# Performance work log

Measured on AMD Instinct MI355X. Metric: run time of the kernel, lower is better.

Reference implementation:

```python
import jax, jax.numpy as jnp
import numpy as np

DIM = 1024
N_HEADS = 16
HEAD_DIM = DIM // N_HEADS
LN_EPS = 1e-5


def layer_norm(x, gamma, beta):
    mu = jnp.mean(x, axis=-1, keepdims=True)
    var = jnp.var(x, axis=-1, keepdims=True)
    return (x - mu) * jax.lax.rsqrt(var + LN_EPS) * gamma + beta


def setup_inputs() -> dict:
    key = jax.random.key(0)
    ks = jax.random.split(key, 12)
    B, Nq, Nc, D = 2, 2048, 2048, DIM
    s = 1.0 / np.sqrt(D)
    return {
        "query": jax.random.normal(ks[0], (B, Nq, D), jnp.float32),
        "context": jax.random.normal(ks[1], (B, Nc, D), jnp.float32),
        "Wq": jax.random.normal(ks[2], (D, D), jnp.float32) * s,
        "bq": jnp.zeros((D,), jnp.float32),
        "Wk": jax.random.normal(ks[3], (D, D), jnp.float32) * s,
        "bk": jnp.zeros((D,), jnp.float32),
        "Wv": jax.random.normal(ks[4], (D, D), jnp.float32) * s,
        "bv": jnp.zeros((D,), jnp.float32),
        "Wo": jax.random.normal(ks[5], (D, D), jnp.float32) * s,
        "bo": jnp.zeros((D,), jnp.float32),
        "gq": jnp.ones((D,), jnp.float32),
        "betaq": jnp.zeros((D,), jnp.float32),
        "gkv": jnp.ones((D,), jnp.float32),
        "betakv": jnp.zeros((D,), jnp.float32),
    }


def reference(query, context, Wq, bq, Wk, bk, Wv, bv, Wo, bo, gq, betaq, gkv, betakv):
    B, Nq, D = query.shape
    Nc = context.shape[1]
    residual = query
    q = layer_norm(query, gq, betaq)
    c = layer_norm(context, gkv, betakv)
    # projections; (B,N,D) -> (B,H,N,hd)
    Q = (q @ Wq + bq).reshape(B, Nq, N_HEADS, HEAD_DIM).transpose(0, 2, 1, 3)
    K = (c @ Wk + bk).reshape(B, Nc, N_HEADS, HEAD_DIM).transpose(0, 2, 1, 3)
    V = (c @ Wv + bv).reshape(B, Nc, N_HEADS, HEAD_DIM).transpose(0, 2, 1, 3)
    scores = jnp.einsum("bhqd,bhkd->bhqk", Q, K) / np.sqrt(HEAD_DIM).astype(np.float32)
    attn = jax.nn.softmax(scores, axis=-1)
    out = jnp.einsum("bhqk,bhkd->bhqd", attn, V)
    out = out.transpose(0, 2, 1, 3).reshape(B, Nq, D)
    return residual + out @ Wo + bo
```

## Files before the change

### kernel.cpp

```cpp
#include <hip/hip_runtime.h>
#include <hip/hip_bf16.h>

typedef unsigned short u16;
typedef unsigned long long u64;
typedef __bf16 bf16x8 __attribute__((ext_vector_type(8)));
typedef float f32x4 __attribute__((ext_vector_type(4)));
typedef float f32x16 __attribute__((ext_vector_type(16)));
typedef unsigned u32x4 __attribute__((ext_vector_type(4)));

#define DIM 1024
#define NH 16
#define HD 64
#define QSCALE 0.180336880972788f

__device__ __forceinline__ u16 f2bf(float f) {
  union { float f; unsigned u; } v; v.f = f;
  unsigned r = v.u + 0x7fffu + ((v.u >> 16) & 1u);
  return (u16)(r >> 16);
}

__device__ __forceinline__ unsigned pk2(float a, float b) {
  union { __hip_bfloat162 h; unsigned u; } cv;
  cv.h = __float22bfloat162_rn(make_float2(a, b));
  return cv.u;
}

__device__ __forceinline__ float bf2f(unsigned s) {
  union { unsigned u; float f; } v; v.u = s << 16; return v.f;
}

__device__ __forceinline__ float fexp2(float x) {
#if __has_builtin(__builtin_amdgcn_exp2f)
  return __builtin_amdgcn_exp2f(x);
#else
  return exp2f(x);
#endif
}

__device__ __forceinline__ void gld16(const u16* gp, u16* lp) {
  __builtin_amdgcn_global_load_lds(
      (const __attribute__((address_space(1))) unsigned int*)(const void*)gp,
      (__attribute__((address_space(3))) unsigned int*)(void*)lp, 16, 0, 0);
}

__device__ __forceinline__ void pl32swap(unsigned& a, unsigned& b) {
  asm volatile("v_permlane32_swap_b32 %0, %1" : "+v"(a), "+v"(b));
}

__device__ __forceinline__ void drain_vm_barrier() {
  asm volatile("s_waitcnt vmcnt(0)" ::: "memory");
  __builtin_amdgcn_s_barrier();
}

__global__ __launch_bounds__(256) void prep_kernel(
    const float* __restrict__ q, const float* __restrict__ c,
    const float* __restrict__ gq, const float* __restrict__ bq,
    const float* __restrict__ gkv, const float* __restrict__ bkv,
    u16* __restrict__ qn, u16* __restrict__ cn,
    const float* W0, const float* W1, const float* W2, const float* W3,
    u16* O0, u16* O1, u16* O2, u16* O3) {
  __shared__ float red[2][4];
  __shared__ float t[32][33];
  int bid = blockIdx.x, tid = threadIdx.x;
  if (bid < 8192) {
    const float* x  = bid < 4096 ? q : c;
    const float* g  = bid < 4096 ? gq : gkv;
    const float* be = bid < 4096 ? bq : bkv;
    u16* out = bid < 4096 ? qn : cn;
    int row = bid & 4095;
    float4 v = ((const float4*)(x + (size_t)row * DIM))[tid];
    float s1 = v.x + v.y + v.z + v.w;
    float s2 = v.x * v.x + v.y * v.y + v.z * v.z + v.w * v.w;
#pragma unroll
    for (int o = 32; o >= 1; o >>= 1) { s1 += __shfl_xor(s1, o, 64); s2 += __shfl_xor(s2, o, 64); }
    int wv = tid >> 6;
    if ((tid & 63) == 0) { red[0][wv] = s1; red[1][wv] = s2; }
    __syncthreads();
    s1 = red[0][0] + red[0][1] + red[0][2] + red[0][3];
    s2 = red[1][0] + red[1][1] + red[1][2] + red[1][3];
    float mu = s1 * (1.f / DIM);
    float var = s2 * (1.f / DIM) - mu * mu;
    float rs = rsqrtf(var + 1e-5f);
    float4 gv = ((const float4*)g)[tid];
    float4 bv = ((const float4*)be)[tid];
    uint2 o2;
    o2.x = pk2((v.x - mu) * rs * gv.x + bv.x, (v.y - mu) * rs * gv.y + bv.y);
    o2.y = pk2((v.z - mu) * rs * gv.z + bv.z, (v.w - mu) * rs * gv.w + bv.w);
    ((uint2*)(out + (size_t)row * DIM))[tid] = o2;
  } else {
    int wid = bid - 8192;
    int z = wid >> 10;
    const float* W = z == 0 ? W0 : z == 1 ? W1 : z == 2 ? W2 : W3;
    u16* O        = z == 0 ? O0 : z == 1 ? O1 : z == 2 ? O2 : O3;
    int xy = wid & 1023;
    int bx = (xy & 31) * 32, by = (xy >> 5) * 32;
    int tx = tid & 31, ty = tid >> 5;
#pragma unroll
    for (int i = 0; i < 4; ++i) t[ty + i * 8][tx] = W[(size_t)(by + ty + i * 8) * DIM + bx + tx];
    __syncthreads();
#pragma unroll
    for (int i = 0; i < 4; ++i) O[(size_t)(bx + ty + i * 8) * DIM + by + tx] = f2bf(t[tx][ty + i * 8]);
  }
}

#define QKV_BUF 16384
__global__ __launch_bounds__(256) void gemm_qkv(
    const u16* __restrict__ qn, const u16* __restrict__ cn,
    const u16* __restrict__ Wqt, const u16* __restrict__ Wkt, const u16* __restrict__ Wvt,
    const float* __restrict__ bq, const float* __restrict__ bk, const float* __restrict__ bv,
    u16* __restrict__ Qb, u16* __restrict__ Kb, u16* __restrict__ Vtb) {
  __shared__ __align__(16) u16 sm[2 * QKV_BUF];
  int tid = threadIdx.x, wave = tid >> 6, lane = tid & 63;
  int lr = lane & 15, quad = lane >> 4;
  int m0 = blockIdx.x * 128, n0 = blockIdx.y * 64;
  int wm = (wave >> 1) * 64, wn = (wave & 1) * 32;

  if (blockIdx.z == 0) {
    auto stage = [&](int buf, int kt) {
      u16* As  = sm + buf * QKV_BUF;
      u16* B0s = As + 128 * 64;
      u16* B1s = As + 192 * 64;
#pragma unroll
      for (int r = 0; r < 4; ++r) {
        int slot = tid + r * 256;
        int row = slot >> 3;
        int c = (slot & 7) ^ (row & 7);
        gld16(cn + (size_t)(m0 + row) * DIM + kt + c * 8, &As[slot * 8]);
      }
#pragma unroll
      for (int r = 0; r < 2; ++r) {
        int slot = tid + r * 256;
        int row = slot >> 3;
        int c = (slot & 7) ^ (row & 7);
        gld16(Wkt + (size_t)(n0 + row) * DIM + kt + c * 8, &B0s[slot * 8]);
        gld16(Wvt + (size_t)(n0 + row) * DIM + kt + c * 8, &B1s[slot * 8]);
      }
    };

    f32x4 acck[4][2] = {}, accv[4][2] = {};
    stage(0, 0);
    drain_vm_barrier();
    int cur = 0;
    for (int kt = 0; kt < DIM; kt += 64) {
      if (kt + 64 < DIM) stage(cur ^ 1, kt + 64);
      const u16* As  = sm + cur * QKV_BUF;
      const u16* B0s = As + 128 * 64;
      const u16* B1s = As + 192 * 64;
#pragma unroll
      for (int kc = 0; kc < 2; ++kc) {
        int pc = ((kc * 4 + quad) ^ (lr & 7)) * 8;
        bf16x8 af[4], b0f[2], b1f[2];
#pragma unroll
        for (int i = 0; i < 4; ++i) af[i] = *(const bf16x8*)&As[(wm + i * 16 + lr) * 64 + pc];
#pragma unroll
        for (int j = 0; j < 2; ++j) {
          b0f[j] = *(const bf16x8*)&B0s[(wn + j * 16 + lr) * 64 + pc];
          b1f[j] = *(const bf16x8*)&B1s[(wn + j * 16 + lr) * 64 + pc];
        }
#pragma unroll
        for (int mi = 0; mi < 4; ++mi)
#pragma unroll
          for (int ni = 0; ni < 2; ++ni) {
            acck[mi][ni] = __builtin_amdgcn_mfma_f32_16x16x32_bf16(af[mi], b0f[ni], acck[mi][ni], 0, 0, 0);
            accv[mi][ni] = __builtin_amdgcn_mfma_f32_16x16x32_bf16(b1f[ni], af[mi], accv[mi][ni], 0, 0, 0);
          }
      }
      drain_vm_barrier();
      cur ^= 1;
    }
#pragma unroll
    for (int mi = 0; mi < 4; ++mi)
#pragma unroll
      for (int ni = 0; ni < 2; ++ni) {
        int col = n0 + wn + ni * 16 + lr;
        float bb_ = bk[col];
        int row0 = m0 + wm + mi * 16 + quad * 4;
#pragma unroll
        for (int r = 0; r < 4; ++r)
          Kb[(size_t)(row0 + r) * DIM + col] = f2bf(acck[mi][ni][r] + bb_);
      }
#pragma unroll
    for (int mi = 0; mi < 4; ++mi) {
      int m = m0 + wm + mi * 16 + lr;
      int bb = m >> 11, tt = m & 2047;
      u16* outb = Vtb + (((size_t)bb << 10)) * 2048 + tt;
#pragma unroll
      for (int ni = 0; ni < 2; ++ni) {
        int nbase = n0 + wn + ni * 16 + quad * 4;
#pragma unroll
        for (int r = 0; r < 4; ++r)
          outb[(size_t)(nbase + r) * 2048] = f2bf(accv[mi][ni][r] + bv[nbase + r]);
      }
    }
  } else {
    auto stage = [&](int buf, int kt) {
      u16* As  = sm + buf * QKV_BUF;
      u16* B0s = As + 128 * 64;
#pragma unroll
      for (int r = 0; r < 4; ++r) {
        int slot = tid + r * 256;
        int row = slot >> 3;
        int c = (slot & 7) ^ (row & 7);
        gld16(qn + (size_t)(m0 + row) * DIM + kt + c * 8, &As[slot * 8]);
      }
#pragma unroll
      for (int r = 0; r < 2; ++r) {
        int slot = tid + r * 256;
        int row = slot >> 3;
        int c = (slot & 7) ^ (row & 7);
        gld16(Wqt + (size_t)(n0 + row) * DIM + kt + c * 8, &B0s[slot * 8]);
      }
    };

    f32x4 acc[4][2] = {};
    stage(0, 0);
    drain_vm_barrier();
    int cur = 0;
    for (int kt = 0; kt < DIM; kt += 64) {
      if (kt + 64 < DIM) stage(cur ^ 1, kt + 64);
      const u16* As  = sm + cur * QKV_BUF;
      const u16* B0s = As + 128 * 64;
#pragma unroll
      for (int kc = 0; kc < 2; ++kc) {
        int pc = ((kc * 4 + quad) ^ (lr & 7)) * 8;
        bf16x8 af[4], b0f[2];
#pragma unroll
        for (int i = 0; i < 4; ++i) af[i] = *(const bf16x8*)&As[(wm + i * 16 + lr) * 64 + pc];
#pragma unroll
        for (int j = 0; j < 2; ++j) b0f[j] = *(const bf16x8*)&B0s[(wn + j * 16 + lr) * 64 + pc];
#pragma unroll
        for (int mi = 0; mi < 4; ++mi)
#pragma unroll
          for (int ni = 0; ni < 2; ++ni)
            acc[mi][ni] = __builtin_amdgcn_mfma_f32_16x16x32_bf16(af[mi], b0f[ni], acc[mi][ni], 0, 0, 0);
      }
      drain_vm_barrier();
      cur ^= 1;
    }
#pragma unroll
    for (int mi = 0; mi < 4; ++mi)
#pragma unroll
      for (int ni = 0; ni < 2; ++ni) {
        int col = n0 + wn + ni * 16 + lr;
        float bb_ = bq[col];
        int row0 = m0 + wm + mi * 16 + quad * 4;
#pragma unroll
        for (int r = 0; r < 4; ++r)
          Qb[(size_t)(row0 + r) * DIM + col] = f2bf((acc[mi][ni][r] + bb_) * QSCALE);
      }
  }
}

#define O_BUF 12288
__global__ __launch_bounds__(256) void gemm_o(const u16* __restrict__ A,
    const u16* __restrict__ Bt, const float* __restrict__ bias,
    float* __restrict__ out, const float* __restrict__ resid) {
  __shared__ __align__(16) u16 sm[2 * O_BUF];
  int tid = threadIdx.x, wave = tid >> 6, lane = tid & 63;
  int lr = lane & 15, quad = lane >> 4;
  int m0 = blockIdx.x * 128, n0 = blockIdx.y * 64;
  int wm = (wave >> 1) * 64, wn = (wave & 1) * 32;

  auto stage = [&](int buf, int kt) {
    u16* As = sm + buf * O_BUF;
    u16* Bs = As + 128 * 64;
#pragma unroll
    for (int r = 0; r < 4; ++r) {
      int slot = tid + r * 256;
      int row = slot >> 3;
      int c = (slot & 7) ^ (row & 7);
      gld16(A + (size_t)(m0 + row) * DIM + kt + c * 8, &As[slot * 8]);
    }
#pragma unroll
    for (int r = 0; r < 2; ++r) {
      int slot = tid + r * 256;
      int row = slot >> 3;
      int c = (slot & 7) ^ (row & 7);
      gld16(Bt + (size_t)(n0 + row) * DIM + kt + c * 8, &Bs[slot * 8]);
    }
  };

  f32x4 acc[4][2] = {};
  stage(0, 0);
  drain_vm_barrier();
  int cur = 0;
  for (int kt = 0; kt < DIM; kt += 64) {
    if (kt + 64 < DIM) stage(cur ^ 1, kt + 64);
    const u16* As = sm + cur * O_BUF;
    const u16* Bs = As + 128 * 64;
#pragma unroll
    for (int kc = 0; kc < 2; ++kc) {
      int pc = ((kc * 4 + quad) ^ (lr & 7)) * 8;
      bf16x8 af[4], bfr[2];
#pragma unroll
      for (int i = 0; i < 4; ++i) af[i] = *(const bf16x8*)&As[(wm + i * 16 + lr) * 64 + pc];
#pragma unroll
      for (int j = 0; j < 2; ++j) bfr[j] = *(const bf16x8*)&Bs[(wn + j * 16 + lr) * 64 + pc];
#pragma unroll
      for (int mi = 0; mi < 4; ++mi)
#pragma unroll
        for (int ni = 0; ni < 2; ++ni)
          acc[mi][ni] = __builtin_amdgcn_mfma_f32_16x16x32_bf16(af[mi], bfr[ni], acc[mi][ni], 0, 0, 0);
    }
    drain_vm_barrier();
    cur ^= 1;
  }
#pragma unroll
  for (int mi = 0; mi < 4; ++mi)
#pragma unroll
    for (int ni = 0; ni < 2; ++ni) {
      int col = n0 + wn + ni * 16 + lr;
      float bv = bias[col];
      int row0 = m0 + wm + mi * 16 + quad * 4;
#pragma unroll
      for (int r = 0; r < 4; ++r) {
        int row = row0 + r;
        out[(size_t)row * DIM + col] = acc[mi][ni][r] + bv + resid[(size_t)row * DIM + col];
      }
    }
}

__global__ __launch_bounds__(256, 4) void flash_kernel(const u16* __restrict__ Q,
    const u16* __restrict__ Kg, const u16* __restrict__ Vt,
    u16* __restrict__ O0, u16* __restrict__ O1,
    float* __restrict__ L0, float* __restrict__ L1) {
  __shared__ __align__(16) u16 lds[16384];
  int tid = threadIdx.x, wave = tid >> 6, lane = tid & 63;
  int ln = lane & 31, hi = lane >> 5;
  int bh = blockIdx.x, b = bh >> 4, h = bh & 15;
  int q0 = blockIdx.y * 128;
  int split = blockIdx.z;
  u16* Op = split ? O1 : O0;
  float* Lp = split ? L1 : L0;
  int t0 = split * 1024;

  const u16* kbase = Kg + (size_t)(b * 2048 + t0) * DIM + h * HD;
  const u16* vbase = Vt + (size_t)(b * 1024 + h * HD) * 2048 + t0;

  size_t qrow = (size_t)(b * 2048 + q0 + wave * 32 + ln);
  bf16x8 qf[4];
#pragma unroll
  for (int ds = 0; ds < 4; ++ds)
    qf[ds] = *(const bf16x8*)&Q[qrow * DIM + h * HD + ds * 16 + hi * 8];

  int slot0 = tid, slot1 = tid + 256;
  int r0 = slot0 >> 3, c0 = (slot0 & 7) ^ (r0 & 7);
  int r1 = slot1 >> 3, c1 = (slot1 & 7) ^ (r1 & 7);
  const u16* kp0 = kbase + (size_t)r0 * DIM + c0 * 8;
  const u16* kp1 = kbase + (size_t)r1 * DIM + c1 * 8;
  const u16* vp0 = vbase + (size_t)r0 * 2048 + c0 * 8;
  const u16* vp1 = vbase + (size_t)r1 * 2048 + c1 * 8;

  gld16(kp0, &lds[slot0 * 8]);
  gld16(kp1, &lds[slot1 * 8]);
  gld16(vp0, &lds[8192 + slot0 * 8]);
  gld16(vp1, &lds[8192 + slot1 * 8]);
  __syncthreads();

  float plsum = 0.f;
  f32x16 oacc[2] = {};

  for (int j = 0; j < 16; ++j) {
    int par = j & 1;
    const u16* kcb = &lds[par * 4096];
    const u16* vcb = &lds[8192 + par * 4096];

    f32x16 sf[2] = {};
    __builtin_amdgcn_s_setprio(1);
#pragma unroll
    for (int kt2 = 0; kt2 < 2; ++kt2) {
      int rs = (kt2 * 32 + ln) * 64;
      int rx = (kt2 * 32 + ln) & 7;
#pragma unroll
      for (int ds = 0; ds < 4; ++ds) {
        bf16x8 kf = *(const bf16x8*)&kcb[rs + (((ds * 2 + hi) ^ rx) * 8)];
        sf[kt2] = __builtin_amdgcn_mfma_f32_32x32x16_bf16(kf, qf[ds], sf[kt2], 0, 0, 0);
      }
    }
    __builtin_amdgcn_s_setprio(0);

    if (j < 15) {
      int np = par ^ 1;
      kp0 += 64 * DIM; kp1 += 64 * DIM; vp0 += 64; vp1 += 64;
      gld16(kp0, &lds[np * 4096 + slot0 * 8]);
      gld16(kp1, &lds[np * 4096 + slot1 * 8]);
      gld16(vp0, &lds[8192 + np * 4096 + slot0 * 8]);
      gld16(vp1, &lds[8192 + np * 4096 + slot1 * 8]);
    }

    bf16x8 pb[4];
#pragma unroll
    for (int kt2 = 0; kt2 < 2; ++kt2)
#pragma unroll
      for (int ks = 0; ks < 2; ++ks) {
        float e0 = fexp2(sf[kt2][ks * 8 + 0]), e1 = fexp2(sf[kt2][ks * 8 + 1]);
        float e2 = fexp2(sf[kt2][ks * 8 + 2]), e3 = fexp2(sf[kt2][ks * 8 + 3]);
        float e4 = fexp2(sf[kt2][ks * 8 + 4]), e5 = fexp2(sf[kt2][ks * 8 + 5]);
        float e6 = fexp2(sf[kt2][ks * 8 + 6]), e7 = fexp2(sf[kt2][ks * 8 + 7]);
        plsum += ((e0 + e1) + (e2 + e3)) + ((e4 + e5) + (e6 + e7));
        unsigned w0 = pk2(e0, e1), w1 = pk2(e2, e3);
        unsigned w2 = pk2(e4, e5), w3 = pk2(e6, e7);
        pl32swap(w0, w2);
        pl32swap(w1, w3);
        u32x4 t; t.x = w0; t.y = w1; t.z = w2; t.w = w3;
        pb[kt2 * 2 + ks] = __builtin_bit_cast(bf16x8, t);
      }

    __builtin_amdgcn_s_setprio(1);
#pragma unroll
    for (int dt = 0; dt < 2; ++dt) {
      int rs = (dt * 32 + ln) * 64;
      int rx = (dt * 32 + ln) & 7;
#pragma unroll
      for (int kk = 0; kk < 4; ++kk) {
        bf16x8 vf = *(const bf16x8*)&vcb[rs + (((kk * 2 + hi) ^ rx) * 8)];
        oacc[dt] = __builtin_amdgcn_mfma_f32_32x32x16_bf16(vf, pb[kk], oacc[dt], 0, 0, 0);
      }
    }
    __builtin_amdgcn_s_setprio(0);
    __syncthreads();
  }

  float l = plsum + __shfl_xor(plsum, 32, 64);
  if (hi == 0) Lp[qrow * 16 + h] = l;
#pragma unroll
  for (int dt = 0; dt < 2; ++dt)
#pragma unroll
    for (int g = 0; g < 4; ++g) {
      uint2 pk;
      pk.x = pk2(oacc[dt][g * 4 + 0], oacc[dt][g * 4 + 1]);
      pk.y = pk2(oacc[dt][g * 4 + 2], oacc[dt][g * 4 + 3]);
      *(uint2*)&Op[qrow * DIM + h * HD + dt * 32 + g * 8 + hi * 4] = pk;
    }
}

__global__ __launch_bounds__(256) void combine_kernel(const u16* __restrict__ O0,
    const u16* __restrict__ O1, const float* __restrict__ L0, const float* __restrict__ L1,
    u16* __restrict__ AO) {
  int row = blockIdx.x, tid = threadIdx.x;
  int h = tid >> 4;
  float rl = 1.f / (L0[row * 16 + h] + L1[row * 16 + h]);
  uint2 a = ((const uint2*)(O0 + (size_t)row * DIM))[tid];
  uint2 b = ((const uint2*)(O1 + (size_t)row * DIM))[tid];
  float v0 = (bf2f(a.x & 0xffff) + bf2f(b.x & 0xffff)) * rl;
  float v1 = (bf2f(a.x >> 16)    + bf2f(b.x >> 16))    * rl;
  float v2 = (bf2f(a.y & 0xffff) + bf2f(b.y & 0xffff)) * rl;
  float v3 = (bf2f(a.y >> 16)    + bf2f(b.y >> 16))    * rl;
  uint2 o;
  o.x = pk2(v0, v1);
  o.y = pk2(v2, v3);
  ((uint2*)(AO + (size_t)row * DIM))[tid] = o;
}

extern "C" void kernel_launch(void* const* d_in, const int* in_sizes, int n_in,
                              void* d_out, int out_size, void* d_ws, size_t ws_size,
                              hipStream_t stream) {
  const float* query   = (const float*)d_in[0];
  const float* context = (const float*)d_in[1];
  const float* Wq = (const float*)d_in[2];
  const float* bq = (const float*)d_in[3];
  const float* Wk = (const float*)d_in[4];
  const float* bk = (const float*)d_in[5];
  const float* Wv = (const float*)d_in[6];
  const float* bv = (const float*)d_in[7];
  const float* Wo = (const float*)d_in[8];
  const float* bo = (const float*)d_in[9];
  const float* gq    = (const float*)d_in[10];
  const float* betaq = (const float*)d_in[11];
  const float* gkv   = (const float*)d_in[12];
  const float* betakv= (const float*)d_in[13];
  (void)in_sizes; (void)n_in; (void)out_size; (void)ws_size;

  char* ws = (char*)d_ws;
  const size_t MB = (size_t)1 << 20;
  u16* qn  = (u16*)(ws + 0 * MB);
  u16* cn  = (u16*)(ws + 8 * MB);
  u16* Wqt = (u16*)(ws + 16 * MB);
  u16* Wkt = (u16*)(ws + 18 * MB);
  u16* Wvt = (u16*)(ws + 20 * MB);
  u16* Wot = (u16*)(ws + 22 * MB);
  u16* Qb  = (u16*)(ws + 24 * MB);
  u16* Kb  = (u16*)(ws + 32 * MB);
  u16* Vtb = (u16*)(ws + 40 * MB);
  u16* AOb = (u16*)(ws + 48 * MB);
  u16* Op0 = qn;
  u16* Op1 = cn;
  float* L0 = (float*)(ws + 16 * MB);
  float* L1 = (float*)(ws + 16 * MB + 256 * 1024);

  prep_kernel<<<12288, 256, 0, stream>>>(query, context, gq, betaq, gkv, betakv,
                                         qn, cn, Wq, Wk, Wv, Wo, Wqt, Wkt, Wvt, Wot);

  gemm_qkv<<<dim3(32, 16, 2), 256, 0, stream>>>(qn, cn, Wqt, Wkt, Wvt,
                                                bq, bk, bv, Qb, Kb, Vtb);

  flash_kernel<<<dim3(32, 16, 2), 256, 0, stream>>>(Qb, Kb, Vtb, Op0, Op1, L0, L1);

  combine_kernel<<<4096, 256, 0, stream>>>(Op0, Op1, L0, L1, AOb);

  gemm_o<<<dim3(32, 16), 256, 0, stream>>>(AOb, Wot, bo, (float*)d_out, query);
}
```

Before: 204.6 us.

## Drop split-KV flash attention and combine kernel; use 4-slot LDS ring

Removes the two-way key split, so each block walks all 2048 keys and normalizes its output in place. This makes the separate combine kernel and its partial-output and L round trips through memory unnecessary. The K/V staging becomes a four-slot LDS ring that prefetches two tiles ahead with one barrier per pair of tiles, and LDS per block doubles. The cost is half as many blocks (512) and a lower occupancy hint, which risks less latency hiding on a large GPU.

```diff
diff --git a/kernel.cpp b/kernel.cpp
--- a/kernel.cpp
+++ b/kernel.cpp
@@ -320,22 +320,16 @@
     }
 }
 
-__global__ __launch_bounds__(256, 4) void flash_kernel(const u16* __restrict__ Q,
-    const u16* __restrict__ Kg, const u16* __restrict__ Vt,
-    u16* __restrict__ O0, u16* __restrict__ O1,
-    float* __restrict__ L0, float* __restrict__ L1) {
-  __shared__ __align__(16) u16 lds[16384];
+__global__ __launch_bounds__(256, 2) void flash_kernel(const u16* __restrict__ Q,
+    const u16* __restrict__ Kg, const u16* __restrict__ Vt, u16* __restrict__ AO) {
+  __shared__ __align__(16) u16 lds[32768];
   int tid = threadIdx.x, wave = tid >> 6, lane = tid & 63;
   int ln = lane & 31, hi = lane >> 5;
   int bh = blockIdx.x, b = bh >> 4, h = bh & 15;
   int q0 = blockIdx.y * 128;
-  int split = blockIdx.z;
-  u16* Op = split ? O1 : O0;
-  float* Lp = split ? L1 : L0;
-  int t0 = split * 1024;
-
-  const u16* kbase = Kg + (size_t)(b * 2048 + t0) * DIM + h * HD;
-  const u16* vbase = Vt + (size_t)(b * 1024 + h * HD) * 2048 + t0;
+
+  const u16* kbase = Kg + (size_t)(b * 2048) * DIM + h * HD;
+  const u16* vbase = Vt + (size_t)(b * 1024 + h * HD) * 2048;
 
   size_t qrow = (size_t)(b * 2048 + q0 + wave * 32 + ln);
   bf16x8 qf[4];
@@ -351,105 +345,97 @@
   const u16* vp0 = vbase + (size_t)r0 * 2048 + c0 * 8;
   const u16* vp1 = vbase + (size_t)r1 * 2048 + c1 * 8;
 
-  gld16(kp0, &lds[slot0 * 8]);
-  gld16(kp1, &lds[slot1 * 8]);
-  gld16(vp0, &lds[8192 + slot0 * 8]);
-  gld16(vp1, &lds[8192 + slot1 * 8]);
-  __syncthreads();
+#pragma unroll
+  for (int t = 0; t < 2; ++t) {
+    gld16(kp0, &lds[t * 4096 + slot0 * 8]);
+    gld16(kp1, &lds[t * 4096 + slot1 * 8]);
+    gld16(vp0, &lds[16384 + t * 4096 + slot0 * 8]);
+    gld16(vp1, &lds[16384 + t * 4096 + slot1 * 8]);
+    kp0 += 64 * DIM; kp1 += 64 * DIM; vp0 += 64; vp1 += 64;
+  }
+  drain_vm_barrier();
 
   float plsum = 0.f;
   f32x16 oacc[2] = {};
 
-  for (int j = 0; j < 16; ++j) {
-    int par = j & 1;
-    const u16* kcb = &lds[par * 4096];
-    const u16* vcb = &lds[8192 + par * 4096];
-
-    f32x16 sf[2] = {};
-    __builtin_amdgcn_s_setprio(1);
-#pragma unroll
-    for (int kt2 = 0; kt2 < 2; ++kt2) {
-      int rs = (kt2 * 32 + ln) * 64;
-      int rx = (kt2 * 32 + ln) & 7;
-#pragma unroll
-      for (int ds = 0; ds < 4; ++ds) {
-        bf16x8 kf = *(const bf16x8*)&kcb[rs + (((ds * 2 + hi) ^ rx) * 8)];
-        sf[kt2] = __builtin_amdgcn_mfma_f32_32x32x16_bf16(kf, qf[ds], sf[kt2], 0, 0, 0);
-      }
-    }
-    __builtin_amdgcn_s_setprio(0);
-
-    if (j < 15) {
-      int np = par ^ 1;
-      kp0 += 64 * DIM; kp1 += 64 * DIM; vp0 += 64; vp1 += 64;
-      gld16(kp0, &lds[np * 4096 + slot0 * 8]);
-      gld16(kp1, &lds[np * 4096 + slot1 * 8]);
-      gld16(vp0, &lds[8192 + np * 4096 + slot0 * 8]);
-      gld16(vp1, &lds[8192 + np * 4096 + slot1 * 8]);
-    }
-
-    bf16x8 pb[4];
-#pragma unroll
-    for (int kt2 = 0; kt2 < 2; ++kt2)
-#pragma unroll
-      for (int ks = 0; ks < 2; ++ks) {
-        float e0 = fexp2(sf[kt2][ks * 8 + 0]), e1 = fexp2(sf[kt2][ks * 8 + 1]);
-        float e2 = fexp2(sf[kt2][ks * 8 + 2]), e3 = fexp2(sf[kt2][ks * 8 + 3]);
-        float e4 = fexp2(sf[kt2][ks * 8 + 4]), e5 = fexp2(sf[kt2][ks * 8 + 5]);
-        float e6 = fexp2(sf[kt2][ks * 8 + 6]), e7 = fexp2(sf[kt2][ks * 8 + 7]);
-        plsum += ((e0 + e1) + (e2 + e3)) + ((e4 + e5) + (e6 + e7));
-        unsigned w0 = pk2(e0, e1), w1 = pk2(e2, e3);
-        unsigned w2 = pk2(e4, e5), w3 = pk2(e6, e7);
-        pl32swap(w0, w2);
-        pl32swap(w1, w3);
-        u32x4 t; t.x = w0; t.y = w1; t.z = w2; t.w = w3;
-        pb[kt2 * 2 + ks] = __builtin_bit_cast(bf16x8, t);
-      }
-
-    __builtin_amdgcn_s_setprio(1);
-#pragma unroll
-    for (int dt = 0; dt < 2; ++dt) {
-      int rs = (dt * 32 + ln) * 64;
-      int rx = (dt * 32 + ln) & 7;
-#pragma unroll
-      for (int kk = 0; kk < 4; ++kk) {
-        bf16x8 vf = *(const bf16x8*)&vcb[rs + (((kk * 2 + hi) ^ rx) * 8)];
-        oacc[dt] = __builtin_amdgcn_mfma_f32_32x32x16_bf16(vf, pb[kk], oacc[dt], 0, 0, 0);
-      }
-    }
-    __builtin_amdgcn_s_setprio(0);
-    __syncthreads();
+  for (int j = 0; j < 32; j += 2) {
+    if (j + 2 < 32) {
+#pragma unroll
+      for (int t = 0; t < 2; ++t) {
+        int bi = (j + 2 + t) & 3;
+        gld16(kp0, &lds[bi * 4096 + slot0 * 8]);
+        gld16(kp1, &lds[bi * 4096 + slot1 * 8]);
+        gld16(vp0, &lds[16384 + bi * 4096 + slot0 * 8]);
+        gld16(vp1, &lds[16384 + bi * 4096 + slot1 * 8]);
+        kp0 += 64 * DIM; kp1 += 64 * DIM; vp0 += 64; vp1 += 64;
+      }
+    }
+
+#pragma unroll
+    for (int jj = 0; jj < 2; ++jj) {
+      int bi = (j + jj) & 3;
+      const u16* kcb = &lds[bi * 4096];
+      const u16* vcb = &lds[16384 + bi * 4096];
+
+      f32x16 sf[2] = {};
+      __builtin_amdgcn_s_setprio(1);
+#pragma unroll
+      for (int kt2 = 0; kt2 < 2; ++kt2) {
+        int rs = (kt2 * 32 + ln) * 64;
+        int rx = (kt2 * 32 + ln) & 7;
+#pragma unroll
+        for (int ds = 0; ds < 4; ++ds) {
+          bf16x8 kf = *(const bf16x8*)&kcb[rs + (((ds * 2 + hi) ^ rx) * 8)];
+          sf[kt2] = __builtin_amdgcn_mfma_f32_32x32x16_bf16(kf, qf[ds], sf[kt2], 0, 0, 0);
+        }
+      }
+      __builtin_amdgcn_s_setprio(0);
+
+      bf16x8 pb[4];
+#pragma unroll
+      for (int kt2 = 0; kt2 < 2; ++kt2)
+#pragma unroll
+        for (int ks = 0; ks < 2; ++ks) {
+          float e0 = fexp2(sf[kt2][ks * 8 + 0]), e1 = fexp2(sf[kt2][ks * 8 + 1]);
+          float e2 = fexp2(sf[kt2][ks * 8 + 2]), e3 = fexp2(sf[kt2][ks * 8 + 3]);
+          float e4 = fexp2(sf[kt2][ks * 8 + 4]), e5 = fexp2(sf[kt2][ks * 8 + 5]);
+          float e6 = fexp2(sf[kt2][ks * 8 + 6]), e7 = fexp2(sf[kt2][ks * 8 + 7]);
+          plsum += ((e0 + e1) + (e2 + e3)) + ((e4 + e5) + (e6 + e7));
+          unsigned w0 = pk2(e0, e1), w1 = pk2(e2, e3);
+          unsigned w2 = pk2(e4, e5), w3 = pk2(e6, e7);
+          pl32swap(w0, w2);
+          pl32swap(w1, w3);
+          u32x4 t; t.x = w0; t.y = w1; t.z = w2; t.w = w3;
+          pb[kt2 * 2 + ks] = __builtin_bit_cast(bf16x8, t);
+        }
+
+      __builtin_amdgcn_s_setprio(1);
+#pragma unroll
+      for (int dt = 0; dt < 2; ++dt) {
+        int rs = (dt * 32 + ln) * 64;
+        int rx = (dt * 32 + ln) & 7;
+#pragma unroll
+        for (int kk = 0; kk < 4; ++kk) {
+          bf16x8 vf = *(const bf16x8*)&vcb[rs + (((kk * 2 + hi) ^ rx) * 8)];
+          oacc[dt] = __builtin_amdgcn_mfma_f32_32x32x16_bf16(vf, pb[kk], oacc[dt], 0, 0, 0);
+        }
+      }
+      __builtin_amdgcn_s_setprio(0);
+    }
+    drain_vm_barrier();
   }
 
   float l = plsum + __shfl_xor(plsum, 32, 64);
-  if (hi == 0) Lp[qrow * 16 + h] = l;
+  float rl = 1.f / l;
 #pragma unroll
   for (int dt = 0; dt < 2; ++dt)
 #pragma unroll
     for (int g = 0; g < 4; ++g) {
       uint2 pk;
-      pk.x = pk2(oacc[dt][g * 4 + 0], oacc[dt][g * 4 + 1]);
-      pk.y = pk2(oacc[dt][g * 4 + 2], oacc[dt][g * 4 + 3]);
-      *(uint2*)&Op[qrow * DIM + h * HD + dt * 32 + g * 8 + hi * 4] = pk;
-    }
-}
-
-__global__ __launch_bounds__(256) void combine_kernel(const u16* __restrict__ O0,
-    const u16* __restrict__ O1, const float* __restrict__ L0, const float* __restrict__ L1,
-    u16* __restrict__ AO) {
-  int row = blockIdx.x, tid = threadIdx.x;
-  int h = tid >> 4;
-  float rl = 1.f / (L0[row * 16 + h] + L1[row * 16 + h]);
-  uint2 a = ((const uint2*)(O0 + (size_t)row * DIM))[tid];
-  uint2 b = ((const uint2*)(O1 + (size_t)row * DIM))[tid];
-  float v0 = (bf2f(a.x & 0xffff) + bf2f(b.x & 0xffff)) * rl;
-  float v1 = (bf2f(a.x >> 16)    + bf2f(b.x >> 16))    * rl;
-  float v2 = (bf2f(a.y & 0xffff) + bf2f(b.y & 0xffff)) * rl;
-  float v3 = (bf2f(a.y >> 16)    + bf2f(b.y >> 16))    * rl;
-  uint2 o;
-  o.x = pk2(v0, v1);
-  o.y = pk2(v2, v3);
-  ((uint2*)(AO + (size_t)row * DIM))[tid] = o;
+      pk.x = pk2(oacc[dt][g * 4 + 0] * rl, oacc[dt][g * 4 + 1] * rl);
+      pk.y = pk2(oacc[dt][g * 4 + 2] * rl, oacc[dt][g * 4 + 3] * rl);
+      *(uint2*)&AO[qrow * DIM + h * HD + dt * 32 + g * 8 + hi * 4] = pk;
+    }
 }
 
 extern "C" void kernel_launch(void* const* d_in, const int* in_sizes, int n_in,
@@ -483,10 +469,6 @@
   u16* Kb  = (u16*)(ws + 32 * MB);
   u16* Vtb = (u16*)(ws + 40 * MB);
   u16* AOb = (u16*)(ws + 48 * MB);
-  u16* Op0 = qn;
-  u16* Op1 = cn;
-  float* L0 = (float*)(ws + 16 * MB);
-  float* L1 = (float*)(ws + 16 * MB + 256 * 1024);
 
   prep_kernel<<<12288, 256, 0, stream>>>(query, context, gq, betaq, gkv, betakv,
                                          qn, cn, Wq, Wk, Wv, Wo, Wqt, Wkt, Wvt, Wot);
@@ -494,9 +476,7 @@
   gemm_qkv<<<dim3(32, 16, 2), 256, 0, stream>>>(qn, cn, Wqt, Wkt, Wvt,
                                                 bq, bk, bv, Qb, Kb, Vtb);
 
-  flash_kernel<<<dim3(32, 16, 2), 256, 0, stream>>>(Qb, Kb, Vtb, Op0, Op1, L0, L1);
-
-  combine_kernel<<<4096, 256, 0, stream>>>(Op0, Op1, L0, L1, AOb);
+  flash_kernel<<<dim3(32, 16), 256, 0, stream>>>(Qb, Kb, Vtb, AOb);
 
   gemm_o<<<dim3(32, 16), 256, 0, stream>>>(AOb, Wot, bo, (float*)d_out, query);
 }
```

Result: no change. 203.0 us (median of 3 runs) (-0.8%).
